# Performance work log

Measured on AMD Instinct MI355X. Metric: run time of the kernel, lower is better.

Reference implementation:

```python
import jax, jax.numpy as jnp
import numpy as np

LN_EPS = 1e-6


def setup_inputs() -> dict:
    key = jax.random.key(0)
    ks = jax.random.split(key, 8)
    B, T, V, r, c, D = 1, 2048, 50257, 16, 16, 1024
    rc = r * c
    return {
        "input_ids": jax.random.randint(ks[0], (B, T), 0, V),
        "token_to_mu_w": jax.random.normal(ks[1], (rc, V), jnp.float32) * 0.02,  # nn.Linear(V, rc).weight
        "pos_embedding": jax.random.normal(ks[2], (1, T, r, c), jnp.float32) * 0.02,
        "w1": jax.random.normal(ks[3], (D, rc), jnp.float32) * 0.05,  # Linear(rc, D).weight
        "b1": jnp.zeros((D,), jnp.float32),
        "ln_w": jnp.ones((D,), jnp.float32),
        "ln_b": jnp.zeros((D,), jnp.float32),
        "w2": jax.random.normal(ks[4], (V, D), jnp.float32) * 0.02,  # Linear(D, V).weight
        "b2": jnp.zeros((V,), jnp.float32),
    }


def reference(input_ids, token_to_mu_w, pos_embedding, w1, b1, ln_w, ln_b, w2, b2):
    B, T = input_ids.shape
    r, c = pos_embedding.shape[2], pos_embedding.shape[3]
    # one_hot(input_ids) @ W^T is exactly a row-gather of W^T (single nonzero per row)
    MU = jnp.take(token_to_mu_w.T, input_ids, axis=0)          # [B, T, rc]
    MU = MU.reshape(B, T, r, c) + pos_embedding[:, :T]         # [B, T, r, c]
    # n_layers = 0: no transformer blocks; dropout is identity in eval
    x = MU.reshape(B, T, r * c)
    h = jax.nn.gelu(jnp.einsum('btk,dk->btd', x, w1) + b1, approximate=False)
    mean = jnp.mean(h, axis=-1, keepdims=True)
    var = jnp.mean(jnp.square(h - mean), axis=-1, keepdims=True)
    h = (h - mean) * jax.lax.rsqrt(var + LN_EPS) * ln_w + ln_b
    logits = jnp.einsum('btd,vd->btv', h, w2) + b2             # [B, T, V]
    return logits, MU
```

## Files before the change

### kernel.cpp

```cpp
#include <hip/hip_runtime.h>
#include <hip/hip_bf16.h>
#include <math.h>

#define T_LEN 2048
#define RC 256
#define DIM 1024
#define VOCAB 50257
#define NT 32
#define SLOT 4096

using short8 = __attribute__((ext_vector_type(8))) short;
using f32x4  = __attribute__((ext_vector_type(4))) float;

#define VMCNT(n) asm volatile("s_waitcnt vmcnt(" #n ")" ::: "memory")
#define SCHED_FENCE() __builtin_amdgcn_sched_barrier(0)

__device__ __forceinline__ unsigned short f2bf(float f) {
    unsigned int u = __float_as_uint(f);
    u += 0x7fffu + ((u >> 16) & 1u);
    return (unsigned short)(u >> 16);
}

__device__ __forceinline__ void async_load16(void* lds, const void* g) {
    __builtin_amdgcn_global_load_lds(
        (const __attribute__((address_space(1))) void*)g,
        (__attribute__((address_space(3))) void*)lds,
        16, 0, 0);
}

__global__ __launch_bounds__(256) void mu_kernel(
    const int* __restrict__ ids, const float* __restrict__ tokw,
    const float* __restrict__ pos, float* __restrict__ mu) {
    int t = blockIdx.x, k = threadIdx.x;
    int id = ids[t];
    float v = tokw[(size_t)k * VOCAB + id] + pos[t * RC + k];
    mu[t * RC + k] = v;
}

__global__ __launch_bounds__(256) void gemm1_gelu_kernel(
    const float* __restrict__ mu, const float* __restrict__ w1,
    const float* __restrict__ b1, float* __restrict__ hpre) {
    __shared__ float xs[16][RC];
    const int tg = blockIdx.x, ng = blockIdx.y, tid = threadIdx.x;
    const int t0 = tg * 16;
    {
        const float4* src = (const float4*)(mu + (size_t)t0 * RC);
        float4* dst = (float4*)&xs[0][0];
        #pragma unroll
        for (int i = 0; i < 4; ++i) dst[tid + 256 * i] = src[tid + 256 * i];
    }
    __syncthreads();
    const int d = ng * 256 + tid;
    float acc[16];
    const float bias = b1[d];
    #pragma unroll
    for (int t = 0; t < 16; ++t) acc[t] = bias;
    const float4* w1r = (const float4*)(w1 + (size_t)d * RC);
    for (int k4 = 0; k4 < RC / 4; ++k4) {
        const float4 w = w1r[k4];
        #pragma unroll
        for (int t = 0; t < 16; ++t) {
            const float4 xv = *(const float4*)&xs[t][k4 * 4];
            acc[t] += w.x * xv.x + w.y * xv.y + w.z * xv.z + w.w * xv.w;
        }
    }
    #pragma unroll
    for (int t = 0; t < 16; ++t) {
        float x = acc[t];
        float g = 0.5f * x * (1.0f + erff(x * 0.70710678118654752f));
        hpre[(size_t)(t0 + t) * DIM + d] = g;
    }
}

__global__ __launch_bounds__(256) void ln_kernel(
    const float* __restrict__ hpre, const float* __restrict__ lnw,
    const float* __restrict__ lnb, unsigned short* __restrict__ h) {
    const int t = blockIdx.x, tid = threadIdx.x;
    const float4 v = ((const float4*)(hpre + (size_t)t * DIM))[tid];
    float s  = v.x + v.y + v.z + v.w;
    float ss = v.x * v.x + v.y * v.y + v.z * v.z + v.w * v.w;
    #pragma unroll
    for (int off = 32; off > 0; off >>= 1) {
        s  += __shfl_down(s, off, 64);
        ss += __shfl_down(ss, off, 64);
    }
    __shared__ float red[8];
    const int wid = tid >> 6, lane = tid & 63;
    if (lane == 0) { red[wid] = s; red[4 + wid] = ss; }
    __syncthreads();
    const float S  = red[0] + red[1] + red[2] + red[3];
    const float SS = red[4] + red[5] + red[6] + red[7];
    const float mean = S * (1.0f / DIM);
    const float var  = SS * (1.0f / DIM) - mean * mean;
    const float inv  = 1.0f / sqrtf(var + 1e-6f);
    const float4 wv = ((const float4*)lnw)[tid];
    const float4 bv = ((const float4*)lnb)[tid];
    ushort4 o;
    o.x = f2bf((v.x - mean) * inv * wv.x + bv.x);
    o.y = f2bf((v.y - mean) * inv * wv.y + bv.y);
    o.z = f2bf((v.z - mean) * inv * wv.z + bv.z);
    o.w = f2bf((v.w - mean) * inv * wv.w + bv.w);
    ((ushort4*)h)[(size_t)t * (DIM / 4) + tid] = o;
}

__global__ __launch_bounds__(256) void cvt_kernel(
    const float* __restrict__ src, unsigned short* __restrict__ dst, int n4) {
    int i = blockIdx.x * 256 + threadIdx.x;
    const int stride = gridDim.x * 256;
    for (; i < n4; i += stride) {
        const float4 v = ((const float4*)src)[i];
        ushort4 o;
        o.x = f2bf(v.x); o.y = f2bf(v.y); o.z = f2bf(v.z); o.w = f2bf(v.w);
        ((ushort4*)dst)[i] = o;
    }
}

__device__ __forceinline__ void stage_tile(
    const unsigned short* __restrict__ A, const unsigned short* __restrict__ B,
    unsigned short* As_s, unsigned short* Bs_s,
    int m0, int n0, int kt, int tid, int lk_src) {
    #pragma unroll
    for (int p = 0; p < 2; ++p) {
        const int g = p * 256 + tid;
        const int row = g >> 2;
        async_load16(As_s + (size_t)g * 8,
                     A + (size_t)(m0 + row) * DIM + kt * 32 + lk_src * 8);
    }
    #pragma unroll
    for (int p = 0; p < 2; ++p) {
        const int g = p * 256 + tid;
        const int row = g >> 2;
        int bn = n0 + row; if (bn > VOCAB - 1) bn = VOCAB - 1;
        async_load16(Bs_s + (size_t)g * 8,
                     B + (size_t)bn * DIM + kt * 32 + lk_src * 8);
    }
}

__global__ __launch_bounds__(256, 3) void gemm2_kernel(
    const unsigned short* __restrict__ A, const unsigned short* __restrict__ B,
    const float* __restrict__ b2, float* __restrict__ out) {
    __shared__ unsigned short As[3 * SLOT];
    __shared__ unsigned short Bs[3 * SLOT];

    const int tid  = threadIdx.x;
    const int cpx  = gridDim.x >> 3;
    const int wgid = (blockIdx.x & 7) * cpx + (blockIdx.x >> 3);
    const int m0   = (wgid & 15) << 7;
    const int n0   = (wgid >> 4) << 7;

    const int lane = tid & 63;
    const int lr   = lane & 15;
    const int lk   = lane >> 4;
    const int wid  = tid >> 6;
    const int wr   = wid >> 1;
    const int wc   = wid & 1;
    const int xr     = (lk ^ ((lr >> 1) & 3)) * 8;
    const int arow0  = wr * 64 + lr;
    const int brow0  = wc * 64 + lr;
    const int lk_src = (tid & 3) ^ ((tid >> 3) & 3);

    f32x4 acc[4][4];
    #pragma unroll
    for (int m = 0; m < 4; ++m)
        #pragma unroll
        for (int n = 0; n < 4; ++n) acc[m][n] = {0.f, 0.f, 0.f, 0.f};

    stage_tile(A, B, As, Bs, m0, n0, 0, tid, lk_src);
    SCHED_FENCE();
    stage_tile(A, B, As + SLOT, Bs + SLOT, m0, n0, 1, tid, lk_src);
    SCHED_FENCE();
    VMCNT(4);
    __builtin_amdgcn_s_barrier();

    int cur = 0, st2 = 2;
    #pragma unroll 1
    for (int t = 0; t < NT; ++t) {
        const unsigned short* As_t = As + cur * SLOT;
        const unsigned short* Bs_t = Bs + cur * SLOT;
        short8 af[4], bf[4];
        #pragma unroll
        for (int m = 0; m < 4; ++m)
            af[m] = *(const short8*)(As_t + (arow0 + m * 16) * 32 + xr);
        #pragma unroll
        for (int n = 0; n < 4; ++n)
            bf[n] = *(const short8*)(Bs_t + (brow0 + n * 16) * 32 + xr);
        if (t + 2 < NT)
            stage_tile(A, B, As + st2 * SLOT, Bs + st2 * SLOT, m0, n0, t + 2, tid, lk_src);
        SCHED_FENCE();
        if (t < NT - 2) { VMCNT(4); } else { VMCNT(0); }
        __builtin_amdgcn_s_barrier();
        __builtin_amdgcn_s_setprio(1);
        #pragma unroll
        for (int m = 0; m < 4; ++m)
            #pragma unroll
            for (int n = 0; n < 4; ++n)
                acc[m][n] = __builtin_amdgcn_mfma_f32_16x16x32_bf16(
                    af[m], bf[n], acc[m][n], 0, 0, 0);
        __builtin_amdgcn_s_setprio(0);
        SCHED_FENCE();
        __builtin_amdgcn_s_barrier();
        if (++cur == 3) cur = 0;
        if (++st2 == 3) st2 = 0;
    }

    float bias[4]; int col[4]; bool ok[4];
    #pragma unroll
    for (int n = 0; n < 4; ++n) {
        col[n] = n0 + wc * 64 + n * 16 + lr;
        ok[n]  = col[n] < VOCAB;
        bias[n] = ok[n] ? b2[col[n]] : 0.f;
    }
    #pragma unroll
    for (int m = 0; m < 4; ++m) {
        const int row = m0 + wr * 64 + m * 16 + lk * 4;
        #pragma unroll
        for (int n = 0; n < 4; ++n) {
            if (ok[n]) {
                #pragma unroll
                for (int j = 0; j < 4; ++j)
                    out[(size_t)(row + j) * VOCAB + col[n]] = acc[m][n][j] + bias[n];
            }
        }
    }
}

extern "C" void kernel_launch(void* const* d_in, const int* in_sizes, int n_in,
                              void* d_out, int out_size, void* d_ws, size_t ws_size,
                              hipStream_t stream) {
    (void)in_sizes; (void)n_in; (void)out_size; (void)ws_size;
    const int*   ids  = (const int*)d_in[0];
    const float* tokw = (const float*)d_in[1];
    const float* pos  = (const float*)d_in[2];
    const float* w1   = (const float*)d_in[3];
    const float* b1   = (const float*)d_in[4];
    const float* lnw  = (const float*)d_in[5];
    const float* lnb  = (const float*)d_in[6];
    const float* w2   = (const float*)d_in[7];
    const float* b2   = (const float*)d_in[8];

    float* logits = (float*)d_out;
    float* mu_out = logits + (size_t)T_LEN * VOCAB;

    unsigned short* w2b = (unsigned short*)d_ws;
    unsigned short* hb  = (unsigned short*)((char*)d_ws + (size_t)VOCAB * DIM * 2);
    float* hpre = logits;

    mu_kernel<<<dim3(T_LEN), dim3(256), 0, stream>>>(ids, tokw, pos, mu_out);
    gemm1_gelu_kernel<<<dim3(T_LEN / 16, DIM / 256), dim3(256), 0, stream>>>(
        mu_out, w1, b1, hpre);
    ln_kernel<<<dim3(T_LEN), dim3(256), 0, stream>>>(hpre, lnw, lnb, hb);
    cvt_kernel<<<dim3(2048), dim3(256), 0, stream>>>(
        w2, w2b, (int)((size_t)VOCAB * DIM / 4));
    const int ntiles_n = (VOCAB + 127) / 128;
    gemm2_kernel<<<dim3(16 * ntiles_n), dim3(256), 0, stream>>>(hb, w2b, b2, logits);
}
```

Measured before the change: 476.6 us.

## Fuse fp32-to-bf16 conversion of w2 into the logits GEMM B-tile staging

Removes the standalone pass that converts the whole w2 matrix to bf16 in workspace. The logits GEMM now loads fp32 w2 tiles into registers two steps ahead and converts them to bf16 when writing the swizzled shared-memory tile. The A operand keeps its async global-to-LDS path, and the main loop is unrolled by two to alternate register buffers. This drops a full read-write pass over w2, but each GEMM tile now pulls twice the bytes for B and holds more registers, which may strain occupancy and L2 bandwidth.

```diff
diff --git a/kernel.cpp b/kernel.cpp
--- a/kernel.cpp
+++ b/kernel.cpp
@@ -9,10 +9,12 @@
 #define NT 32
 #define SLOT 4096
 
-using short8 = __attribute__((ext_vector_type(8))) short;
-using f32x4  = __attribute__((ext_vector_type(4))) float;
+using short8  = __attribute__((ext_vector_type(8))) short;
+using ushort8 = __attribute__((ext_vector_type(8))) unsigned short;
+using f32x4   = __attribute__((ext_vector_type(4))) float;
 
 #define VMCNT(n) asm volatile("s_waitcnt vmcnt(" #n ")" ::: "memory")
+#define LGKMCNT0() asm volatile("s_waitcnt lgkmcnt(0)" ::: "memory")
 #define SCHED_FENCE() __builtin_amdgcn_sched_barrier(0)
 
 __device__ __forceinline__ unsigned short f2bf(float f) {
@@ -103,22 +105,11 @@
     ((ushort4*)h)[(size_t)t * (DIM / 4) + tid] = o;
 }
 
-__global__ __launch_bounds__(256) void cvt_kernel(
-    const float* __restrict__ src, unsigned short* __restrict__ dst, int n4) {
-    int i = blockIdx.x * 256 + threadIdx.x;
-    const int stride = gridDim.x * 256;
-    for (; i < n4; i += stride) {
-        const float4 v = ((const float4*)src)[i];
-        ushort4 o;
-        o.x = f2bf(v.x); o.y = f2bf(v.y); o.z = f2bf(v.z); o.w = f2bf(v.w);
-        ((ushort4*)dst)[i] = o;
-    }
-}
-
-__device__ __forceinline__ void stage_tile(
-    const unsigned short* __restrict__ A, const unsigned short* __restrict__ B,
-    unsigned short* As_s, unsigned short* Bs_s,
-    int m0, int n0, int kt, int tid, int lk_src) {
+struct BReg { float4 v0, v1, v2, v3; };
+
+__device__ __forceinline__ void stage_A(
+    const unsigned short* __restrict__ A, unsigned short* As_s,
+    int m0, int kt, int tid, int lk_src) {
     #pragma unroll
     for (int p = 0; p < 2; ++p) {
         const int g = p * 256 + tid;
@@ -126,18 +117,80 @@
         async_load16(As_s + (size_t)g * 8,
                      A + (size_t)(m0 + row) * DIM + kt * 32 + lk_src * 8);
     }
-    #pragma unroll
-    for (int p = 0; p < 2; ++p) {
-        const int g = p * 256 + tid;
-        const int row = g >> 2;
-        int bn = n0 + row; if (bn > VOCAB - 1) bn = VOCAB - 1;
-        async_load16(Bs_s + (size_t)g * 8,
-                     B + (size_t)bn * DIM + kt * 32 + lk_src * 8);
-    }
-}
+}
+
+__device__ __forceinline__ void load_breg(
+    const float* __restrict__ B, int n0, int kt, int tid, BReg& r) {
+    const int g    = tid & 3;
+    const int row0 = tid >> 2;
+    int r0 = n0 + row0;       if (r0 > VOCAB - 1) r0 = VOCAB - 1;
+    int r1 = n0 + row0 + 64;  if (r1 > VOCAB - 1) r1 = VOCAB - 1;
+    const float* p0 = B + (size_t)r0 * DIM + kt * 32 + g * 8;
+    const float* p1 = B + (size_t)r1 * DIM + kt * 32 + g * 8;
+    r.v0 = ((const float4*)p0)[0]; r.v1 = ((const float4*)p0)[1];
+    r.v2 = ((const float4*)p1)[0]; r.v3 = ((const float4*)p1)[1];
+}
+
+__device__ __forceinline__ void write_breg(
+    unsigned short* Bs_s, int tid, const BReg& r) {
+    const int g = tid & 3, row0 = tid >> 2;
+    {
+        const int row = row0;
+        const int gs  = g ^ ((row >> 1) & 3);
+        ushort8 o;
+        o[0]=f2bf(r.v0.x); o[1]=f2bf(r.v0.y); o[2]=f2bf(r.v0.z); o[3]=f2bf(r.v0.w);
+        o[4]=f2bf(r.v1.x); o[5]=f2bf(r.v1.y); o[6]=f2bf(r.v1.z); o[7]=f2bf(r.v1.w);
+        *(ushort8*)(Bs_s + row * 32 + gs * 8) = o;
+    }
+    {
+        const int row = row0 + 64;
+        const int gs  = g ^ ((row >> 1) & 3);
+        ushort8 o;
+        o[0]=f2bf(r.v2.x); o[1]=f2bf(r.v2.y); o[2]=f2bf(r.v2.z); o[3]=f2bf(r.v2.w);
+        o[4]=f2bf(r.v3.x); o[5]=f2bf(r.v3.y); o[6]=f2bf(r.v3.z); o[7]=f2bf(r.v3.w);
+        *(ushort8*)(Bs_s + row * 32 + gs * 8) = o;
+    }
+}
+
+#define GEMM2_BODY(T, WRSET, LDSET)                                            \
+  {                                                                            \
+    const int t_ = (T);                                                        \
+    const unsigned short* As_t = As + cur * SLOT;                              \
+    const unsigned short* Bs_t = Bs + cur * SLOT;                              \
+    const int s1 = (cur == 2) ? 0 : cur + 1;                                   \
+    const int s2 = (cur == 0) ? 2 : cur - 1;                                   \
+    short8 af[4], bf[4];                                                       \
+    _Pragma("unroll")                                                          \
+    for (int m = 0; m < 4; ++m)                                                \
+        af[m] = *(const short8*)(As_t + (arow0 + m * 16) * 32 + xr);           \
+    _Pragma("unroll")                                                          \
+    for (int n = 0; n < 4; ++n)                                                \
+        bf[n] = *(const short8*)(Bs_t + (brow0 + n * 16) * 32 + xr);           \
+    if (t_ + 2 < NT) {                                                         \
+        load_breg(B, n0, t_ + 2, tid, LDSET);                                  \
+        stage_A(A, As + s2 * SLOT, m0, t_ + 2, tid, lk_src);                   \
+    }                                                                          \
+    SCHED_FENCE();                                                             \
+    if (t_ < NT - 2) { VMCNT(6); } else { VMCNT(0); }                          \
+    if (t_ + 1 < NT) write_breg(Bs + s1 * SLOT, tid, WRSET);                   \
+    LGKMCNT0();                                                                \
+    __builtin_amdgcn_s_barrier();                                              \
+    SCHED_FENCE();                                                             \
+    __builtin_amdgcn_s_setprio(1);                                             \
+    _Pragma("unroll")                                                          \
+    for (int m = 0; m < 4; ++m)                                                \
+        _Pragma("unroll")                                                      \
+        for (int n = 0; n < 4; ++n)                                            \
+            acc[m][n] = __builtin_amdgcn_mfma_f32_16x16x32_bf16(               \
+                af[m], bf[n], acc[m][n], 0, 0, 0);                             \
+    __builtin_amdgcn_s_setprio(0);                                             \
+    SCHED_FENCE();                                                             \
+    __builtin_amdgcn_s_barrier();                                              \
+    cur = (cur == 2) ? 0 : cur + 1;                                            \
+  }
 
 __global__ __launch_bounds__(256, 3) void gemm2_kernel(
-    const unsigned short* __restrict__ A, const unsigned short* __restrict__ B,
+    const unsigned short* __restrict__ A, const float* __restrict__ B,
     const float* __restrict__ b2, float* __restrict__ out) {
     __shared__ unsigned short As[3 * SLOT];
     __shared__ unsigned short Bs[3 * SLOT];
@@ -165,42 +218,24 @@
         #pragma unroll
         for (int n = 0; n < 4; ++n) acc[m][n] = {0.f, 0.f, 0.f, 0.f};
 
-    stage_tile(A, B, As, Bs, m0, n0, 0, tid, lk_src);
+    BReg bregA, bregB;
+
+    load_breg(B, n0, 0, tid, bregA);
+    stage_A(A, As, m0, 0, tid, lk_src);
     SCHED_FENCE();
-    stage_tile(A, B, As + SLOT, Bs + SLOT, m0, n0, 1, tid, lk_src);
+    load_breg(B, n0, 1, tid, bregB);
+    stage_A(A, As + SLOT, m0, 1, tid, lk_src);
     SCHED_FENCE();
-    VMCNT(4);
+    VMCNT(6);
+    write_breg(Bs, tid, bregA);
+    LGKMCNT0();
     __builtin_amdgcn_s_barrier();
 
-    int cur = 0, st2 = 2;
+    int cur = 0;
     #pragma unroll 1
-    for (int t = 0; t < NT; ++t) {
-        const unsigned short* As_t = As + cur * SLOT;
-        const unsigned short* Bs_t = Bs + cur * SLOT;
-        short8 af[4], bf[4];
-        #pragma unroll
-        for (int m = 0; m < 4; ++m)
-            af[m] = *(const short8*)(As_t + (arow0 + m * 16) * 32 + xr);
-        #pragma unroll
-        for (int n = 0; n < 4; ++n)
-            bf[n] = *(const short8*)(Bs_t + (brow0 + n * 16) * 32 + xr);
-        if (t + 2 < NT)
-            stage_tile(A, B, As + st2 * SLOT, Bs + st2 * SLOT, m0, n0, t + 2, tid, lk_src);
-        SCHED_FENCE();
-        if (t < NT - 2) { VMCNT(4); } else { VMCNT(0); }
-        __builtin_amdgcn_s_barrier();
-        __builtin_amdgcn_s_setprio(1);
-        #pragma unroll
-        for (int m = 0; m < 4; ++m)
-            #pragma unroll
-            for (int n = 0; n < 4; ++n)
-                acc[m][n] = __builtin_amdgcn_mfma_f32_16x16x32_bf16(
-                    af[m], bf[n], acc[m][n], 0, 0, 0);
-        __builtin_amdgcn_s_setprio(0);
-        SCHED_FENCE();
-        __builtin_amdgcn_s_barrier();
-        if (++cur == 3) cur = 0;
-        if (++st2 == 3) st2 = 0;
+    for (int t = 0; t < NT; t += 2) {
+        GEMM2_BODY(t,     bregB, bregA);
+        GEMM2_BODY(t + 1, bregA, bregB);
     }
 
     float bias[4]; int col[4]; bool ok[4];
@@ -241,16 +276,13 @@
     float* logits = (float*)d_out;
     float* mu_out = logits + (size_t)T_LEN * VOCAB;
 
-    unsigned short* w2b = (unsigned short*)d_ws;
-    unsigned short* hb  = (unsigned short*)((char*)d_ws + (size_t)VOCAB * DIM * 2);
+    unsigned short* hb = (unsigned short*)d_ws;
     float* hpre = logits;
 
     mu_kernel<<<dim3(T_LEN), dim3(256), 0, stream>>>(ids, tokw, pos, mu_out);
     gemm1_gelu_kernel<<<dim3(T_LEN / 16, DIM / 256), dim3(256), 0, stream>>>(
         mu_out, w1, b1, hpre);
     ln_kernel<<<dim3(T_LEN), dim3(256), 0, stream>>>(hpre, lnw, lnb, hb);
-    cvt_kernel<<<dim3(2048), dim3(256), 0, stream>>>(
-        w2, w2b, (int)((size_t)VOCAB * DIM / 4));
     const int ntiles_n = (VOCAB + 127) / 128;
-    gemm2_kernel<<<dim3(16 * ntiles_n), dim3(256), 0, stream>>>(hb, w2b, b2, logits);
-}
+    gemm2_kernel<<<dim3(16 * ntiles_n), dim3(256), 0, stream>>>(hb, w2, b2, logits);
+}
```

Measured after the change: 479.0 us. Within noise of the previous version (+0.5%).
